# Optimization experiments

Hardware: AMD Instinct MI355X
Metric: run time of the kernel (lower is better)

The kernel has to match this reference:

```python
import jax, jax.numpy as jnp
import numpy as np

# Canonical Mamba hyperparams (mamba_ssm defaults for d_model=128)
D_MODEL = 128
D_INNER = 2 * D_MODEL          # expand = 2
D_STATE = 16
D_CONV = 4
DT_RANK = (D_MODEL + 15) // 16  # ceil(d_model/16) = 8
B, N, T = 16, 256, 64
EPS = 1e-5


def setup_inputs() -> dict:
    key = jax.random.key(0)
    ks = jax.random.split(key, 10)
    sc = 0.02
    x = jax.random.normal(ks[0], (B, N, D_MODEL, T), jnp.float32)
    gamma = jnp.ones((D_MODEL,), jnp.float32)
    beta = jnp.zeros((D_MODEL,), jnp.float32)
    W_in = jax.random.normal(ks[1], (D_MODEL, 2 * D_INNER), jnp.float32) * sc
    conv_w = jax.random.normal(ks[2], (D_INNER, D_CONV), jnp.float32) * sc
    conv_b = jnp.zeros((D_INNER,), jnp.float32)
    W_x = jax.random.normal(ks[3], (D_INNER, DT_RANK + 2 * D_STATE), jnp.float32) * sc
    W_dt = jax.random.normal(ks[4], (DT_RANK, D_INNER), jnp.float32) * sc
    b_dt = jax.random.normal(ks[5], (D_INNER,), jnp.float32) * sc
    # S4D-real init: A_log = log(1..d_state), broadcast over channels
    A_log = jnp.log(jnp.broadcast_to(
        jnp.arange(1, D_STATE + 1, dtype=jnp.float32), (D_INNER, D_STATE)))
    Dskip = jnp.ones((D_INNER,), jnp.float32)
    W_out = jax.random.normal(ks[6], (D_INNER, D_MODEL), jnp.float32) * sc
    return dict(x=x, gamma=gamma, beta=beta, W_in=W_in, conv_w=conv_w,
                conv_b=conv_b, W_x=W_x, W_dt=W_dt, b_dt=b_dt,
                A_log=A_log, Dskip=Dskip, W_out=W_out)


def _forward(x, gamma, beta, W_in, conv_w, conv_b, W_x, W_dt, b_dt,
             A_log, Dskip, W_out):
    Bb, Nn, Fd, Tt = x.shape
    # (B,N,F,T) -> (B*N, T, F)
    x_in = x.transpose(0, 1, 3, 2).reshape(Bb * Nn, Tt, Fd)

    # LayerNorm over feature dim
    mu = x_in.mean(-1, keepdims=True)
    var = jnp.mean((x_in - mu) ** 2, axis=-1, keepdims=True)
    u = (x_in - mu) * jax.lax.rsqrt(var + EPS) * gamma + beta

    # Mamba: input projection -> (x, z)
    xz = u @ W_in                                   # (BN,T,2*dI)
    xc, z = jnp.split(xz, 2, axis=-1)

    # Depthwise causal conv1d over time (kernel D_CONV) + SiLU
    xp = jnp.pad(xc, ((0, 0), (D_CONV - 1, 0), (0, 0)))
    xconv = sum(xp[:, k:k + Tt, :] * conv_w[:, k] for k in range(D_CONV)) + conv_b
    xact = jax.nn.silu(xconv)                       # (BN,T,dI)

    # Input-dependent SSM parameters
    dbl = xact @ W_x                                # (BN,T,dt_rank+2*dS)
    dt = dbl[..., :DT_RANK]
    Bm = dbl[..., DT_RANK:DT_RANK + D_STATE]        # (BN,T,dS)
    Cm = dbl[..., DT_RANK + D_STATE:]               # (BN,T,dS)
    delta = jax.nn.softplus(dt @ W_dt + b_dt)       # (BN,T,dI)
    A = -jnp.exp(A_log)                             # (dI,dS)

    # Selective scan over time
    def step(h, inp):
        d, b, c, xt = inp                            # (BN,dI) (BN,dS) (BN,dS) (BN,dI)
        dA = jnp.exp(d[:, :, None] * A)              # (BN,dI,dS)
        h = dA * h + (d * xt)[:, :, None] * b[:, None, :]
        y = jnp.einsum('bis,bs->bi', h, c)
        return h, y

    h0 = jnp.zeros((Bb * Nn, D_INNER, D_STATE), x.dtype)
    seq = (delta.transpose(1, 0, 2), Bm.transpose(1, 0, 2),
           Cm.transpose(1, 0, 2), xact.transpose(1, 0, 2))
    _, ys = jax.lax.scan(step, h0, seq)             # (T,BN,dI)
    y = ys.transpose(1, 0, 2) + xact * Dskip
    y = y * jax.nn.silu(z)
    out = y @ W_out                                 # (BN,T,d_model)

    # Residual (dropout is identity in eval/reference), reshape back
    x_out = out + x_in
    return x_out.reshape(Bb, Nn, Tt, Fd).transpose(0, 1, 3, 2)


def reference(x, gamma, beta, W_in, conv_w, conv_b, W_x, W_dt, b_dt,
              A_log, Dskip, W_out):
    return _forward(x, gamma, beta, W_in, conv_w, conv_b, W_x, W_dt, b_dt,
                    A_log, Dskip, W_out)
```

## Files before the change

### kernel.cpp

```cpp
#include <hip/hip_runtime.h>
#include <stdint.h>

typedef unsigned short ushort_t;
typedef __attribute__((ext_vector_type(8))) short bf16x8;
typedef __attribute__((ext_vector_type(4))) float f32x4;
typedef __attribute__((ext_vector_type(2))) float f32x2;

#define P_CONVW 0
#define P_CONVB 1024
#define P_BDT   1280
#define P_A     1536
#define P_DSKIP 5632
#define P_GAMMA 5888
#define P_BETA  6016
#define P_WDT   6144
#define P_TOT   8192

#define OFFB_WINT   0
#define OFFB_WXT    131072
#define OFFB_WOUTT  163840
#define OFFB_PF     229376
#define OFFB_DYN    262144

__device__ __forceinline__ float b2f(ushort_t u) {
    return __uint_as_float(((unsigned int)u) << 16);
}
__device__ __forceinline__ ushort_t f2b(float f) {
    unsigned int x = __float_as_uint(f);
    return (ushort_t)((x + 0x7fffu + ((x >> 16) & 1u)) >> 16);
}
__device__ __forceinline__ bool is_f32_mode(const void* gamma) {
    return ((const unsigned int*)gamma)[0] == 0x3F800000u;
}
__device__ __forceinline__ float ld_any(const void* p, int idx, bool f32m) {
    return f32m ? ((const float*)p)[idx] : b2f(((const ushort_t*)p)[idx]);
}
__device__ __forceinline__ float silu_f(float v) {
    return v * __builtin_amdgcn_rcpf(1.0f + __expf(-v));
}
__device__ __forceinline__ f32x2 pk_fma(f32x2 a, f32x2 b, f32x2 c) {
    f32x2 d; asm("v_pk_fma_f32 %0, %1, %2, %3" : "=v"(d) : "v"(a), "v"(b), "v"(c)); return d;
}
__device__ __forceinline__ f32x2 pk_mul(f32x2 a, f32x2 b) {
    f32x2 d; asm("v_pk_mul_f32 %0, %1, %2" : "=v"(d) : "v"(a), "v"(b)); return d;
}
__device__ __forceinline__ f32x2 pk_add(f32x2 a, f32x2 b) {
    f32x2 d; asm("v_pk_add_f32 %0, %1, %2" : "=v"(d) : "v"(a), "v"(b)); return d;
}

__global__ __launch_bounds__(256) void prep_kernel(
    const void* __restrict__ gamma, const void* __restrict__ beta,
    const void* __restrict__ W_in,  const void* __restrict__ conv_w,
    const void* __restrict__ conv_b,const void* __restrict__ W_x,
    const void* __restrict__ W_dt,  const void* __restrict__ b_dt,
    const void* __restrict__ A_log, const void* __restrict__ Dskip,
    const void* __restrict__ W_out, char* __restrict__ wsb)
{
    const bool f32m = is_f32_mode(gamma);
    ushort_t* WinT  = (ushort_t*)(wsb + OFFB_WINT);
    ushort_t* WxT   = (ushort_t*)(wsb + OFFB_WXT);
    ushort_t* WoutT = (ushort_t*)(wsb + OFFB_WOUTT);
    float*    pf    = (float*)(wsb + OFFB_PF);
    int idx = blockIdx.x * 256 + threadIdx.x;

    if (idx < 65536) {
        int n = idx >> 7, k = idx & 127;
        WinT[idx] = f2b(ld_any(W_in, k * 512 + n, f32m));
    }
    if (idx < 16384) {
        int n = idx >> 8, k = idx & 255;
        WxT[idx] = (n < 40) ? f2b(ld_any(W_x, k * 40 + n, f32m)) : (ushort_t)0;
    }
    if (idx < 32768) {
        int n = idx >> 8, k = idx & 255;
        WoutT[idx] = f2b(ld_any(W_out, k * 128 + n, f32m));
    }
    if (idx < 1024) pf[P_CONVW + idx] = ld_any(conv_w, idx, f32m);
    if (idx < 4096) pf[P_A + idx]     = -__expf(ld_any(A_log, idx, f32m));
    if (idx < 2048) pf[P_WDT + idx]   = ld_any(W_dt, idx, f32m);
    if (idx < 256) {
        pf[P_CONVB + idx] = ld_any(conv_b, idx, f32m);
        pf[P_BDT + idx]   = ld_any(b_dt, idx, f32m);
        pf[P_DSKIP + idx] = ld_any(Dskip, idx, f32m);
    }
    if (idx < 128) {
        pf[P_GAMMA + idx] = ld_any(gamma, idx, f32m);
        pf[P_BETA + idx]  = ld_any(beta, idx, f32m);
    }
}

__global__ __launch_bounds__(256, 3) void k_lngemm1(
    const void* __restrict__ x_v, const void* __restrict__ gamma_v,
    const float* __restrict__ pf, const ushort_t* __restrict__ WinT,
    ushort_t* __restrict__ xz, int seq_base)
{
    __shared__ __align__(16) float uT[128 * 68];
    __shared__ __align__(16) ushort_t Afr[8192];
    __shared__ float red1[256], red2[256];
    __shared__ float mu_s[64], rs_s[64];

    const int tid = threadIdx.x;
    const int sloc = blockIdx.x;
    const bool f32m = is_f32_mode(gamma_v);
    const size_t seq_off = (size_t)(seq_base + sloc) * 8192;

    {
        int f = tid >> 1, th = tid & 1;
        float* dst = uT + f * 68 + th * 32;
        if (!f32m) {
            const uint4* src = (const uint4*)((const ushort_t*)x_v + seq_off + f * 64 + th * 32);
            #pragma unroll
            for (int i = 0; i < 4; ++i) {
                uint4 qd = src[i];
                *(float4*)(dst + i * 8) = make_float4(
                    __uint_as_float(qd.x << 16), __uint_as_float(qd.x & 0xffff0000u),
                    __uint_as_float(qd.y << 16), __uint_as_float(qd.y & 0xffff0000u));
                *(float4*)(dst + i * 8 + 4) = make_float4(
                    __uint_as_float(qd.z << 16), __uint_as_float(qd.z & 0xffff0000u),
                    __uint_as_float(qd.w << 16), __uint_as_float(qd.w & 0xffff0000u));
            }
        } else {
            const float4* src = (const float4*)((const float*)x_v + seq_off + f * 64 + th * 32);
            #pragma unroll
            for (int i = 0; i < 8; ++i) *(float4*)(dst + i * 4) = src[i];
        }
    }
    __syncthreads();
    {
        int qq = tid >> 6, t = tid & 63;
        float su = 0.f, sq = 0.f;
        #pragma unroll 8
        for (int kk = 0; kk < 32; ++kk) {
            float v = uT[(qq * 32 + kk) * 68 + t];
            su += v; sq += v * v;
        }
        red1[tid] = su; red2[tid] = sq;
    }
    __syncthreads();
    if (tid < 64) {
        float su = red1[tid] + red1[64 + tid] + red1[128 + tid] + red1[192 + tid];
        float sq = red2[tid] + red2[64 + tid] + red2[128 + tid] + red2[192 + tid];
        float mu = su * (1.0f / 128.0f);
        float var = sq * (1.0f / 128.0f) - mu * mu;
        mu_s[tid] = mu;
        rs_s[tid] = rsqrtf(var + 1e-5f);
    }
    __syncthreads();
    {
        int t = tid & 63, dq = tid >> 6;
        float mu = mu_s[t], rs = rs_s[t];
        int mf = t >> 4, r = t & 15;
        #pragma unroll
        for (int k = 0; k < 4; ++k) {
            unsigned int pk4[4];
            #pragma unroll
            for (int e = 0; e < 4; ++e) {
                int d0 = dq * 32 + k * 8 + 2 * e;
                float v0 = (uT[d0 * 68 + t] - mu) * rs * pf[P_GAMMA + d0] + pf[P_BETA + d0];
                float v1 = (uT[(d0 + 1) * 68 + t] - mu) * rs * pf[P_GAMMA + d0 + 1] + pf[P_BETA + d0 + 1];
                pk4[e] = (unsigned int)f2b(v0) | ((unsigned int)f2b(v1) << 16);
            }
            *(uint4*)(Afr + ((dq * 4 + mf) * 64 + k * 16 + r) * 8) =
                make_uint4(pk4[0], pk4[1], pk4[2], pk4[3]);
        }
    }
    __syncthreads();

    {
        const int lane = tid & 63, w = tid >> 6;
        const int r = lane & 15, q = lane >> 4;
        const size_t xzbase = (size_t)sloc * 32768;

        #pragma unroll 1
        for (int nh = 0; nh < 2; ++nh) {
            f32x4 acc[4][4];
            #pragma unroll
            for (int i = 0; i < 4; ++i)
                #pragma unroll
                for (int nf = 0; nf < 4; ++nf) acc[i][nf] = (f32x4)(0.0f);

            #pragma unroll
            for (int ks = 0; ks < 4; ++ks) {
                bf16x8 a[4], b[4];
                #pragma unroll
                for (int i = 0; i < 4; ++i)
                    a[i] = *(const bf16x8*)(Afr + ((ks * 4 + i) * 64 + lane) * 8);
                #pragma unroll
                for (int nf = 0; nf < 4; ++nf) {
                    int n = w * 128 + nh * 64 + nf * 16 + r;
                    b[nf] = *(const bf16x8*)(WinT + (size_t)n * 128 + ks * 32 + q * 8);
                }
                #pragma unroll
                for (int i = 0; i < 4; ++i)
                    #pragma unroll
                    for (int nf = 0; nf < 4; ++nf)
                        acc[i][nf] = __builtin_amdgcn_mfma_f32_16x16x32_bf16(a[i], b[nf], acc[i][nf], 0, 0, 0);
            }
            if (w < 2) {
                #pragma unroll
                for (int i = 0; i < 4; ++i)
                    #pragma unroll
                    for (int nf = 0; nf < 4; ++nf) {
                        int n = w * 128 + nh * 64 + nf * 16 + r;
                        int tb = i * 16 + q * 4;
                        uint2 res;
                        res.x = (unsigned int)f2b(acc[i][nf][0]) |
                                ((unsigned int)f2b(acc[i][nf][1]) << 16);
                        res.y = (unsigned int)f2b(acc[i][nf][2]) |
                                ((unsigned int)f2b(acc[i][nf][3]) << 16);
                        *(uint2*)(xz + xzbase + (size_t)n * 64 + tb) = res;
                    }
            } else {
                #pragma unroll
                for (int i = 0; i < 4; ++i)
                    #pragma unroll
                    for (int nf = 0; nf < 4; ++nf) {
                        int n = w * 128 + nh * 64 + nf * 16 + r;
                        #pragma unroll
                        for (int rg = 0; rg < 4; ++rg) {
                            int trow = i * 16 + q * 4 + rg;
                            xz[xzbase + 16384 + (size_t)trow * 256 + (n - 256)] = f2b(acc[i][nf][rg]);
                        }
                    }
            }
        }
    }
}

__global__ __launch_bounds__(256, 4) void k_fuse(
    const void* __restrict__ x_v, const void* __restrict__ gamma_v,
    const ushort_t* __restrict__ xz, const float* __restrict__ pf,
    const ushort_t* __restrict__ WxT, const ushort_t* __restrict__ WoutT,
    void* __restrict__ out_v, int seq_base)
{
    __shared__ __align__(16) char smem[40960];
    ushort_t* xact_s = (ushort_t*)smem;
    float*    dt_s   = (float*)(smem + 33792);
    ushort_t* BC_s   = (ushort_t*)(smem + 35840);

    const int tid = threadIdx.x;
    const int sloc = blockIdx.x;
    const int sglob = seq_base + sloc;
    const bool f32m = is_f32_mode(gamma_v);
    const int lane = tid & 63, w = tid >> 6;
    const int r = lane & 15, q = lane >> 4;
    const size_t xzbase = (size_t)sloc * 32768;

    {
        const int c = tid;
        float cw0 = pf[P_CONVW + c * 4 + 0], cw1 = pf[P_CONVW + c * 4 + 1];
        float cw2 = pf[P_CONVW + c * 4 + 2], cw3 = pf[P_CONVW + c * 4 + 3];
        float cb  = pf[P_CONVB + c];
        float w0 = 0.f, w1 = 0.f, w2 = 0.f;
        const uint4* xq = (const uint4*)(xz + xzbase + (size_t)c * 64);
        #pragma unroll
        for (int ch = 0; ch < 4; ++ch) {
            uint4 a0 = xq[2 * ch], a1 = xq[2 * ch + 1];
            unsigned int wds[8] = {a0.x, a0.y, a0.z, a0.w, a1.x, a1.y, a1.z, a1.w};
            #pragma unroll
            for (int jj = 0; jj < 8; ++jj) {
                unsigned int v = wds[jj];
                int t = ch * 16 + jj * 2;
                float xv0 = __uint_as_float(v << 16);
                float o0 = cb + w0 * cw0 + w1 * cw1 + w2 * cw2 + xv0 * cw3;
                xact_s[t * 264 + c] = f2b(silu_f(o0));
                w0 = w1; w1 = w2; w2 = xv0;
                float xv1 = __uint_as_float(v & 0xffff0000u);
                float o1 = cb + w0 * cw0 + w1 * cw1 + w2 * cw2 + xv1 * cw3;
                xact_s[(t + 1) * 264 + c] = f2b(silu_f(o1));
                w0 = w1; w1 = w2; w2 = xv1;
            }
        }
    }
    __syncthreads();

    {
        f32x4 acc2[4];
        #pragma unroll
        for (int i = 0; i < 4; ++i) acc2[i] = (f32x4)(0.0f);
        #pragma unroll 1
        for (int ks = 0; ks < 8; ++ks) {
            bf16x8 b = *(const bf16x8*)(WxT + (w * 16 + r) * 256 + ks * 32 + q * 8);
            #pragma unroll
            for (int i = 0; i < 4; ++i) {
                bf16x8 a = *(const bf16x8*)(xact_s + (i * 16 + r) * 264 + ks * 32 + q * 8);
                acc2[i] = __builtin_amdgcn_mfma_f32_16x16x32_bf16(a, b, acc2[i], 0, 0, 0);
            }
        }
        int col = w * 16 + r;
        #pragma unroll
        for (int i = 0; i < 4; ++i)
            #pragma unroll
            for (int rg = 0; rg < 4; ++rg) {
                int trow = i * 16 + q * 4 + rg;
                float v = acc2[i][rg];
                if (col < 8)       dt_s[trow * 8 + col] = v;
                else if (col < 40) BC_s[trow * 40 + (col - 8)] = f2b(v);
            }
    }
    __syncthreads();

    {
        const int i = tid;
        float wdt[8];
        #pragma unroll
        for (int rr = 0; rr < 8; ++rr) wdt[rr] = pf[P_WDT + rr * 256 + i];
        const float bdt = pf[P_BDT + i];
        const float dsk = pf[P_DSKIP + i];

        bool structured = true;
        #pragma unroll
        for (int ss = 0; ss < 16; ++ss) {
            float av = pf[P_A + i * 16 + ss];
            structured = structured && (fabsf(av + (float)(ss + 1)) <= 1e-3f * (float)(ss + 1));
        }

        const ushort_t* zc = xz + xzbase + 16384 + i;

        auto dt_arg = [&](int t) -> float {
            const float* dr = dt_s + t * 8;
            float4 d0 = *(const float4*)dr;
            float4 d1 = *(const float4*)(dr + 4);
            float arg = bdt;
            arg = fmaf(d0.x, wdt[0], arg); arg = fmaf(d0.y, wdt[1], arg);
            arg = fmaf(d0.z, wdt[2], arg); arg = fmaf(d0.w, wdt[3], arg);
            arg = fmaf(d1.x, wdt[4], arg); arg = fmaf(d1.y, wdt[5], arg);
            arg = fmaf(d1.z, wdt[6], arg); arg = fmaf(d1.w, wdt[7], arg);
            return arg;
        };

        if (structured) {
            f32x2 h2[8];
            #pragma unroll
            for (int p = 0; p < 8; ++p) h2[p] = (f32x2){0.f, 0.f};

            f32x2 dAA[8], dAB[8];
            float dxA, xtA, sgA, dxB, xtB, sgB;

            auto PF = [&](int t, f32x2* dA, float& dx, float& xt, float& sg, ushort_t zv) {
                float arg = dt_arg(t);
                float p = __expf(arg);
                float opp = 1.0f + p;
                float e1 = __builtin_amdgcn_rcpf(opp);
                float del = __logf(opp);
                float e2 = e1 * e1, e4 = e2 * e2, e8 = e4 * e4;
                f32x2 m2 = {e2, e2}, m4 = {e4, e4}, m8 = {e8, e8};
                dA[0] = (f32x2){e1, e2};
                dA[1] = pk_mul(dA[0], m2);
                dA[2] = pk_mul(dA[0], m4);
                dA[3] = pk_mul(dA[1], m4);
                dA[4] = pk_mul(dA[0], m8);
                dA[5] = pk_mul(dA[1], m8);
                dA[6] = pk_mul(dA[2], m8);
                dA[7] = pk_mul(dA[3], m8);
                xt = b2f(xact_s[t * 264 + i]);
                dx = del * xt;
                sg = silu_f(b2f(zv));
            };

            auto STEP = [&](int t, const f32x2* dA, float dx, float xt, float sg) -> float {
                const uint4* bq = (const uint4*)(BC_s + t * 40);
                uint4 b0 = bq[0], b1 = bq[1], b2v = bq[2], b3 = bq[3];
                unsigned int pw[16] = {b0.x, b0.y, b0.z, b0.w, b1.x, b1.y, b1.z, b1.w,
                                       b2v.x, b2v.y, b2v.z, b2v.w, b3.x, b3.y, b3.z, b3.w};
                f32x2 dx2 = {dx, dx};
                f32x2 ya = {0.f, 0.f}, yb = {0.f, 0.f};
                #pragma unroll
                for (int p = 0; p < 8; ++p) {
                    unsigned int v = pw[p];
                    f32x2 B2 = {__uint_as_float(v << 16), __uint_as_float(v & 0xffff0000u)};
                    unsigned int vc = pw[8 + p];
                    f32x2 C2 = {__uint_as_float(vc << 16), __uint_as_float(vc & 0xffff0000u)};
                    f32x2 bx = pk_mul(B2, dx2);
                    h2[p] = pk_fma(dA[p], h2[p], bx);
                    if (p & 1) yb = pk_fma(h2[p], C2, yb);
                    else       ya = pk_fma(h2[p], C2, ya);
                }
                f32x2 ys = pk_add(ya, yb);
                float y = ys[0] + ys[1];
                return fmaf(xt, dsk, y) * sg;
            };

            ushort_t z_c = zc[0];
            ushort_t z_n = zc[256];
            PF(0, dAA, dxA, xtA, sgA, z_c);
            z_c = z_n; z_n = zc[2 * 256];

            #pragma unroll 1
            for (int t = 0; t < 64; t += 2) {
                PF(t + 1, dAB, dxB, xtB, sgB, z_c);
                { int tz = (t + 3 > 63) ? 63 : t + 3; z_c = z_n; z_n = zc[tz * 256]; }
                float ygA = STEP(t, dAA, dxA, xtA, sgA);
                int t2 = (t + 2 > 63) ? 63 : t + 2;
                PF(t2, dAA, dxA, xtA, sgA, z_c);
                { int tz = (t + 4 > 63) ? 63 : t + 4; z_c = z_n; z_n = zc[tz * 256]; }
                float ygB = STEP(t + 1, dAB, dxB, xtB, sgB);
                unsigned int pkk;
                asm("v_cvt_pk_bf16_f32 %0, %1, %2" : "=v"(pkk) : "v"(ygA), "v"(ygB));
                xact_s[t * 264 + i] = (ushort_t)(pkk & 0xffffu);
                xact_s[(t + 1) * 264 + i] = (ushort_t)(pkk >> 16);
            }
        } else {
            float Av[16];
            #pragma unroll
            for (int ss = 0; ss < 16; ++ss) Av[ss] = pf[P_A + i * 16 + ss];
            float h[16];
            #pragma unroll
            for (int ss = 0; ss < 16; ++ss) h[ss] = 0.f;
            #pragma unroll 1
            for (int t = 0; t < 64; ++t) {
                float arg = dt_arg(t);
                float delta = __logf(1.0f + __expf(arg));
                unsigned int pk[16];
                const uint2* bq = (const uint2*)(BC_s + t * 40);
                #pragma unroll
                for (int jj = 0; jj < 8; ++jj) {
                    uint2 vv = bq[jj];
                    pk[2 * jj] = vv.x; pk[2 * jj + 1] = vv.y;
                }
                float Bv[16], Cv[16];
                #pragma unroll
                for (int jj = 0; jj < 8; ++jj) {
                    unsigned int v = pk[jj];
                    Bv[2 * jj]     = __uint_as_float(v << 16);
                    Bv[2 * jj + 1] = __uint_as_float(v & 0xffff0000u);
                    unsigned int vc = pk[8 + jj];
                    Cv[2 * jj]     = __uint_as_float(vc << 16);
                    Cv[2 * jj + 1] = __uint_as_float(vc & 0xffff0000u);
                }
                float xt = b2f(xact_s[t * 264 + i]);
                float zf = b2f(zc[t * 256]);
                float dx = delta * xt;
                float y = 0.f;
                #pragma unroll
                for (int ss = 0; ss < 16; ++ss) {
                    float dA = __expf(delta * Av[ss]);
                    h[ss] = fmaf(dA, h[ss], dx * Bv[ss]);
                    y = fmaf(h[ss], Cv[ss], y);
                }
                float yg = fmaf(xt, dsk, y) * silu_f(zf);
                xact_s[t * 264 + i] = f2b(yg);
            }
        }
    }
    __syncthreads();

    {
        f32x4 acc3[4][2];
        #pragma unroll
        for (int i = 0; i < 4; ++i)
            #pragma unroll
            for (int nf = 0; nf < 2; ++nf) acc3[i][nf] = (f32x4)(0.0f);
        #pragma unroll 1
        for (int ks = 0; ks < 8; ++ks) {
            bf16x8 a[4], b[2];
            #pragma unroll
            for (int i = 0; i < 4; ++i)
                a[i] = *(const bf16x8*)(xact_s + (i * 16 + r) * 264 + ks * 32 + q * 8);
            #pragma unroll
            for (int nf = 0; nf < 2; ++nf)
                b[nf] = *(const bf16x8*)(WoutT + (w * 32 + nf * 16 + r) * 256 + ks * 32 + q * 8);
            #pragma unroll
            for (int i = 0; i < 4; ++i)
                #pragma unroll
                for (int nf = 0; nf < 2; ++nf)
                    acc3[i][nf] = __builtin_amdgcn_mfma_f32_16x16x32_bf16(a[i], b[nf], acc3[i][nf], 0, 0, 0);
        }
        if (!f32m) {
            #pragma unroll
            for (int i = 0; i < 4; ++i)
                #pragma unroll
                for (int nf = 0; nf < 2; ++nf) {
                    int d = w * 32 + nf * 16 + r;
                    int tb = i * 16 + q * 4;
                    size_t off = (size_t)sglob * 8192 + (size_t)d * 64 + tb;
                    uint2 xv = *(const uint2*)((const ushort_t*)x_v + off);
                    float x0 = __uint_as_float(xv.x << 16);
                    float x1 = __uint_as_float(xv.x & 0xffff0000u);
                    float x2 = __uint_as_float(xv.y << 16);
                    float x3 = __uint_as_float(xv.y & 0xffff0000u);
                    uint2 res;
                    res.x = (unsigned int)f2b(acc3[i][nf][0] + x0) |
                            ((unsigned int)f2b(acc3[i][nf][1] + x1) << 16);
                    res.y = (unsigned int)f2b(acc3[i][nf][2] + x2) |
                            ((unsigned int)f2b(acc3[i][nf][3] + x3) << 16);
                    *(uint2*)((ushort_t*)out_v + off) = res;
                }
        } else {
            #pragma unroll
            for (int i = 0; i < 4; ++i)
                #pragma unroll
                for (int nf = 0; nf < 2; ++nf) {
                    int d = w * 32 + nf * 16 + r;
                    int tb = i * 16 + q * 4;
                    size_t off = (size_t)sglob * 8192 + (size_t)d * 64 + tb;
                    float4 xv = *(const float4*)((const float*)x_v + off);
                    float4 res = make_float4(acc3[i][nf][0] + xv.x,
                                             acc3[i][nf][1] + xv.y,
                                             acc3[i][nf][2] + xv.z,
                                             acc3[i][nf][3] + xv.w);
                    *(float4*)((float*)out_v + off) = res;
                }
        }
    }
}

extern "C" void kernel_launch(void* const* d_in, const int* in_sizes, int n_in,
                              void* d_out, int out_size, void* d_ws, size_t ws_size,
                              hipStream_t stream)
{
    const void* x      = d_in[0];
    const void* gamma  = d_in[1];
    const void* beta   = d_in[2];
    const void* W_in   = d_in[3];
    const void* conv_w = d_in[4];
    const void* conv_b = d_in[5];
    const void* W_x    = d_in[6];
    const void* W_dt   = d_in[7];
    const void* b_dt   = d_in[8];
    const void* A_log  = d_in[9];
    const void* Dskip  = d_in[10];
    const void* W_out  = d_in[11];

    char* wsb = (char*)d_ws;
    long long avail = (long long)ws_size - OFFB_DYN;
    long long S = avail > 0 ? avail / 65536 : 1;
    if (S > 4096) S = 4096;
    if (S < 1) S = 1;

    ushort_t* WinT  = (ushort_t*)(wsb + OFFB_WINT);
    ushort_t* WxT   = (ushort_t*)(wsb + OFFB_WXT);
    ushort_t* WoutT = (ushort_t*)(wsb + OFFB_WOUTT);
    float*    pf    = (float*)(wsb + OFFB_PF);
    ushort_t* xz_buf= (ushort_t*)(wsb + OFFB_DYN);

    prep_kernel<<<dim3(256), dim3(256), 0, stream>>>(
        gamma, beta, W_in, conv_w, conv_b, W_x, W_dt, b_dt, A_log, Dskip, W_out, wsb);

    for (int base = 0; base < 4096; base += (int)S) {
        int cnt = 4096 - base < (int)S ? 4096 - base : (int)S;
        k_lngemm1<<<dim3(cnt), dim3(256), 0, stream>>>(x, gamma, pf, WinT, xz_buf, base);
        k_fuse<<<dim3(cnt), dim3(256), 0, stream>>>(x, gamma, xz_buf, pf, WxT, WoutT, d_out, base);
    }
}
```

Measured before the change: 709.7 us.

## Fuse LayerNorm+in-proj kernel with scan/out-proj kernel into one launch

Merges the two per-sequence kernels into a single kernel that runs LayerNorm, the input GEMM, the conv/scan and the output GEMM back to back. Shared memory regions are aliased so that one block's buffers fit in about 51 KB. The z half of xz is now written time-contiguous per channel, which lets the scan read two z values per 32-bit load instead of strided single loads. The xz intermediate still goes through global memory (probably L2-resident now) rather than being removed, and the larger shared footprint with launch bounds of 3 may reduce occupancy compared with the old scan kernel.

```diff
diff --git a/kernel.cpp b/kernel.cpp
--- a/kernel.cpp
+++ b/kernel.cpp
@@ -89,20 +89,31 @@
     }
 }
 
-__global__ __launch_bounds__(256, 3) void k_lngemm1(
+__global__ __launch_bounds__(256, 3) void k_mamba(
     const void* __restrict__ x_v, const void* __restrict__ gamma_v,
     const float* __restrict__ pf, const ushort_t* __restrict__ WinT,
-    ushort_t* __restrict__ xz, int seq_base)
+    const ushort_t* __restrict__ WxT, const ushort_t* __restrict__ WoutT,
+    ushort_t* __restrict__ xz, void* __restrict__ out_v, int seq_base)
 {
-    __shared__ __align__(16) float uT[128 * 68];
-    __shared__ __align__(16) ushort_t Afr[8192];
-    __shared__ float red1[256], red2[256];
-    __shared__ float mu_s[64], rs_s[64];
+    __shared__ __align__(16) char smem[51712];
+    float*    uT     = (float*)smem;
+    ushort_t* xact_s = (ushort_t*)smem;
+    ushort_t* Afr    = (ushort_t*)(smem + 34816);
+    float*    red1   = (float*)(smem + 34816);
+    float*    red2   = (float*)(smem + 34816 + 1024);
+    float*    dt_s   = (float*)(smem + 34816);
+    ushort_t* BC_s   = (ushort_t*)(smem + 36864);
+    float*    mu_s   = (float*)(smem + 51200);
+    float*    rs_s   = (float*)(smem + 51456);
 
     const int tid = threadIdx.x;
     const int sloc = blockIdx.x;
+    const int sglob = seq_base + sloc;
     const bool f32m = is_f32_mode(gamma_v);
-    const size_t seq_off = (size_t)(seq_base + sloc) * 8192;
+    const int lane = tid & 63, w = tid >> 6;
+    const int r = lane & 15, q = lane >> 4;
+    const size_t seq_off = (size_t)sglob * 8192;
+    const size_t xzbase = (size_t)sloc * 32768;
 
     {
         int f = tid >> 1, th = tid & 1;
@@ -126,6 +137,7 @@
         }
     }
     __syncthreads();
+
     {
         int qq = tid >> 6, t = tid & 63;
         float su = 0.f, sq = 0.f;
@@ -146,10 +158,11 @@
         rs_s[tid] = rsqrtf(var + 1e-5f);
     }
     __syncthreads();
+
     {
         int t = tid & 63, dq = tid >> 6;
         float mu = mu_s[t], rs = rs_s[t];
-        int mf = t >> 4, r = t & 15;
+        int mf = t >> 4, rr = t & 15;
         #pragma unroll
         for (int k = 0; k < 4; ++k) {
             unsigned int pk4[4];
@@ -160,17 +173,13 @@
                 float v1 = (uT[(d0 + 1) * 68 + t] - mu) * rs * pf[P_GAMMA + d0 + 1] + pf[P_BETA + d0 + 1];
                 pk4[e] = (unsigned int)f2b(v0) | ((unsigned int)f2b(v1) << 16);
             }
-            *(uint4*)(Afr + ((dq * 4 + mf) * 64 + k * 16 + r) * 8) =
+            *(uint4*)(Afr + ((dq * 4 + mf) * 64 + k * 16 + rr) * 8) =
                 make_uint4(pk4[0], pk4[1], pk4[2], pk4[3]);
         }
     }
     __syncthreads();
 
     {
-        const int lane = tid & 63, w = tid >> 6;
-        const int r = lane & 15, q = lane >> 4;
-        const size_t xzbase = (size_t)sloc * 32768;
-
         #pragma unroll 1
         for (int nh = 0; nh < 2; ++nh) {
             f32x4 acc[4][4];
@@ -196,55 +205,22 @@
                     for (int nf = 0; nf < 4; ++nf)
                         acc[i][nf] = __builtin_amdgcn_mfma_f32_16x16x32_bf16(a[i], b[nf], acc[i][nf], 0, 0, 0);
             }
-            if (w < 2) {
-                #pragma unroll
-                for (int i = 0; i < 4; ++i)
-                    #pragma unroll
-                    for (int nf = 0; nf < 4; ++nf) {
-                        int n = w * 128 + nh * 64 + nf * 16 + r;
-                        int tb = i * 16 + q * 4;
-                        uint2 res;
-                        res.x = (unsigned int)f2b(acc[i][nf][0]) |
-                                ((unsigned int)f2b(acc[i][nf][1]) << 16);
-                        res.y = (unsigned int)f2b(acc[i][nf][2]) |
-                                ((unsigned int)f2b(acc[i][nf][3]) << 16);
-                        *(uint2*)(xz + xzbase + (size_t)n * 64 + tb) = res;
-                    }
-            } else {
-                #pragma unroll
-                for (int i = 0; i < 4; ++i)
-                    #pragma unroll
-                    for (int nf = 0; nf < 4; ++nf) {
-                        int n = w * 128 + nh * 64 + nf * 16 + r;
-                        #pragma unroll
-                        for (int rg = 0; rg < 4; ++rg) {
-                            int trow = i * 16 + q * 4 + rg;
-                            xz[xzbase + 16384 + (size_t)trow * 256 + (n - 256)] = f2b(acc[i][nf][rg]);
-                        }
-                    }
-            }
-        }
-    }
-}
-
-__global__ __launch_bounds__(256, 4) void k_fuse(
-    const void* __restrict__ x_v, const void* __restrict__ gamma_v,
-    const ushort_t* __restrict__ xz, const float* __restrict__ pf,
-    const ushort_t* __restrict__ WxT, const ushort_t* __restrict__ WoutT,
-    void* __restrict__ out_v, int seq_base)
-{
-    __shared__ __align__(16) char smem[40960];
-    ushort_t* xact_s = (ushort_t*)smem;
-    float*    dt_s   = (float*)(smem + 33792);
-    ushort_t* BC_s   = (ushort_t*)(smem + 35840);
-
-    const int tid = threadIdx.x;
-    const int sloc = blockIdx.x;
-    const int sglob = seq_base + sloc;
-    const bool f32m = is_f32_mode(gamma_v);
-    const int lane = tid & 63, w = tid >> 6;
-    const int r = lane & 15, q = lane >> 4;
-    const size_t xzbase = (size_t)sloc * 32768;
+            #pragma unroll
+            for (int i = 0; i < 4; ++i)
+                #pragma unroll
+                for (int nf = 0; nf < 4; ++nf) {
+                    int n = w * 128 + nh * 64 + nf * 16 + r;
+                    int tb = i * 16 + q * 4;
+                    uint2 res;
+                    res.x = (unsigned int)f2b(acc[i][nf][0]) |
+                            ((unsigned int)f2b(acc[i][nf][1]) << 16);
+                    res.y = (unsigned int)f2b(acc[i][nf][2]) |
+                            ((unsigned int)f2b(acc[i][nf][3]) << 16);
+                    *(uint2*)(xz + xzbase + (size_t)n * 64 + tb) = res;
+                }
+        }
+    }
+    __syncthreads();
 
     {
         const int c = tid;
@@ -315,7 +291,7 @@
             structured = structured && (fabsf(av + (float)(ss + 1)) <= 1e-3f * (float)(ss + 1));
         }
 
-        const ushort_t* zc = xz + xzbase + 16384 + i;
+        const ushort_t* zrow = xz + xzbase + (size_t)(256 + i) * 64;
 
         auto dt_arg = [&](int t) -> float {
             const float* dr = dt_s + t * 8;
@@ -381,24 +357,24 @@
                 return fmaf(xt, dsk, y) * sg;
             };
 
-            ushort_t z_c = zc[0];
-            ushort_t z_n = zc[256];
-            PF(0, dAA, dxA, xtA, sgA, z_c);
-            z_c = z_n; z_n = zc[2 * 256];
+            const unsigned int* zr = (const unsigned int*)zrow;
+            unsigned int zw_c = zr[0];
+            PF(0, dAA, dxA, xtA, sgA, (ushort_t)(zw_c & 0xffffu));
 
             #pragma unroll 1
             for (int t = 0; t < 64; t += 2) {
-                PF(t + 1, dAB, dxB, xtB, sgB, z_c);
-                { int tz = (t + 3 > 63) ? 63 : t + 3; z_c = z_n; z_n = zc[tz * 256]; }
+                int wn = (t >> 1) + 1; if (wn > 31) wn = 31;
+                unsigned int zw_n = zr[wn];
+                PF(t + 1, dAB, dxB, xtB, sgB, (ushort_t)(zw_c >> 16));
                 float ygA = STEP(t, dAA, dxA, xtA, sgA);
                 int t2 = (t + 2 > 63) ? 63 : t + 2;
-                PF(t2, dAA, dxA, xtA, sgA, z_c);
-                { int tz = (t + 4 > 63) ? 63 : t + 4; z_c = z_n; z_n = zc[tz * 256]; }
+                PF(t2, dAA, dxA, xtA, sgA, (ushort_t)(zw_n & 0xffffu));
                 float ygB = STEP(t + 1, dAB, dxB, xtB, sgB);
                 unsigned int pkk;
                 asm("v_cvt_pk_bf16_f32 %0, %1, %2" : "=v"(pkk) : "v"(ygA), "v"(ygB));
                 xact_s[t * 264 + i] = (ushort_t)(pkk & 0xffffu);
                 xact_s[(t + 1) * 264 + i] = (ushort_t)(pkk >> 16);
+                zw_c = zw_n;
             }
         } else {
             float Av[16];
@@ -429,7 +405,7 @@
                     Cv[2 * jj + 1] = __uint_as_float(vc & 0xffff0000u);
                 }
                 float xt = b2f(xact_s[t * 264 + i]);
-                float zf = b2f(zc[t * 256]);
+                float zf = b2f(zrow[t]);
                 float dx = delta * xt;
                 float y = 0.f;
                 #pragma unroll
@@ -473,7 +449,7 @@
                 for (int nf = 0; nf < 2; ++nf) {
                     int d = w * 32 + nf * 16 + r;
                     int tb = i * 16 + q * 4;
-                    size_t off = (size_t)sglob * 8192 + (size_t)d * 64 + tb;
+                    size_t off = seq_off + (size_t)d * 64 + tb;
                     uint2 xv = *(const uint2*)((const ushort_t*)x_v + off);
                     float x0 = __uint_as_float(xv.x << 16);
                     float x1 = __uint_as_float(xv.x & 0xffff0000u);
@@ -493,7 +469,7 @@
                 for (int nf = 0; nf < 2; ++nf) {
                     int d = w * 32 + nf * 16 + r;
                     int tb = i * 16 + q * 4;
-                    size_t off = (size_t)sglob * 8192 + (size_t)d * 64 + tb;
+                    size_t off = seq_off + (size_t)d * 64 + tb;
                     float4 xv = *(const float4*)((const float*)x_v + off);
                     float4 res = make_float4(acc3[i][nf][0] + xv.x,
                                              acc3[i][nf][1] + xv.y,
@@ -539,7 +515,7 @@
 
     for (int base = 0; base < 4096; base += (int)S) {
         int cnt = 4096 - base < (int)S ? 4096 - base : (int)S;
-        k_lngemm1<<<dim3(cnt), dim3(256), 0, stream>>>(x, gamma, pf, WinT, xz_buf, base);
-        k_fuse<<<dim3(cnt), dim3(256), 0, stream>>>(x, gamma, xz_buf, pf, WxT, WoutT, d_out, base);
-    }
-}
+        k_mamba<<<dim3(cnt), dim3(256), 0, stream>>>(
+            x, gamma, pf, WinT, WxT, WoutT, xz_buf, d_out, base);
+    }
+}
```

Measured after the change: 666.4 us. 6.1% less time.
